# Kernel tuning notes

Hardware: AMD Instinct MI355X
Metric: run time of the kernel (lower is better)

The kernel has to match this reference:

```python
import jax, jax.numpy as jnp
import numpy as np

DIM = 128
H = 8
HD = DIM // H
NL = 6
DFF = 2048
EPS = 1e-5
S2S_STEPS = 6


def _ln(x, g, b):
    m = jnp.mean(x, -1, keepdims=True)
    v = jnp.mean(jnp.square(x - m), -1, keepdims=True)
    return (x - m) / jnp.sqrt(v + EPS) * g + b


def _lstm_step(x, h, c, wih, whh, bih, bhh):
    # torch LSTM gate order: i, f, g, o
    gates = x @ wih.T + bih + h @ whh.T + bhh
    i, f, g, o = jnp.split(gates, 4, axis=-1)
    c = jax.nn.sigmoid(f) * c + jax.nn.sigmoid(i) * jnp.tanh(g)
    h = jax.nn.sigmoid(o) * jnp.tanh(c)
    return h, c


def setup_inputs() -> dict:
    key = jax.random.key(0)
    ks = iter(jax.random.split(key, 16))
    n = lambda shape: jax.random.normal(next(ks), shape, jnp.float32) * 0.02
    inp = {
        "data": jax.random.normal(next(ks), (64, 256, 3), jnp.float32),
        "lin0_w": n((DIM, 3)), "lin0_b": jnp.zeros((DIM,), jnp.float32),
        "attn_in_w": n((NL, 3 * DIM, DIM)), "attn_in_b": jnp.zeros((NL, 3 * DIM), jnp.float32),
        "attn_out_w": n((NL, DIM, DIM)), "attn_out_b": jnp.zeros((NL, DIM), jnp.float32),
        "ln1_g": jnp.ones((NL, DIM), jnp.float32), "ln1_b": jnp.zeros((NL, DIM), jnp.float32),
        "ff_w1": n((NL, DFF, DIM)), "ff_b1": jnp.zeros((NL, DFF), jnp.float32),
        "ff_w2": n((NL, DIM, DFF)), "ff_b2": jnp.zeros((NL, DIM), jnp.float32),
        "ln2_g": jnp.ones((NL, DIM), jnp.float32), "ln2_b": jnp.zeros((NL, DIM), jnp.float32),
        "s2s_wih": n((4 * DIM, 2 * DIM)), "s2s_whh": n((4 * DIM, DIM)),
        "s2s_bih": jnp.zeros((4 * DIM,), jnp.float32), "s2s_bhh": jnp.zeros((4 * DIM,), jnp.float32),
        "mem_wih": n((4 * DIM, 2 * DIM)), "mem_whh": n((4 * DIM, DIM)),
        "mem_bih": jnp.zeros((4 * DIM,), jnp.float32), "mem_bhh": jnp.zeros((4 * DIM,), jnp.float32),
        "lin1_w": n((DIM, DIM)), "lin1_b": jnp.zeros((DIM,), jnp.float32),
        "lin3_w": n((1, DIM)), "lin3_b": jnp.zeros((1,), jnp.float32),
    }
    return inp


def reference(data, lin0_w, lin0_b, attn_in_w, attn_in_b, attn_out_w, attn_out_b,
              ln1_g, ln1_b, ff_w1, ff_b1, ff_w2, ff_b2, ln2_g, ln2_b,
              s2s_wih, s2s_whh, s2s_bih, s2s_bhh,
              mem_wih, mem_whh, mem_bih, mem_bhh,
              lin1_w, lin1_b, lin3_w, lin3_b):
    x = jax.nn.relu(data @ lin0_w.T + lin0_b)  # [S=64, B=256, D]
    S, B, _ = x.shape
    # torch TransformerEncoder with batch_first=False: attention over axis 0,
    # axis 1 is the transformer batch. Post-norm layers (norm_first=False), relu FFN.
    for l in range(NL):
        qkv = x @ attn_in_w[l].T + attn_in_b[l]
        q, k, v = jnp.split(qkv, 3, axis=-1)
        q = q.reshape(S, B, H, HD)
        k = k.reshape(S, B, H, HD)
        v = v.reshape(S, B, H, HD)
        scores = jnp.einsum('sbhd,tbhd->bhst', q, k) / np.float32(np.sqrt(HD))
        attn = jax.nn.softmax(scores, axis=-1)
        ao = jnp.einsum('bhst,tbhd->sbhd', attn, v).reshape(S, B, DIM)
        x = _ln(x + ao @ attn_out_w[l].T + attn_out_b[l], ln1_g[l], ln1_b[l])
        ff = jax.nn.relu(x @ ff_w1[l].T + ff_b1[l]) @ ff_w2[l].T + ff_b2[l]
        x = _ln(x + ff, ln2_g[l], ln2_b[l])
    # Set2Set pooling: bidxs assign segment = axis-0 index for each block of
    # num_atoms consecutive rows of flatten(out,0,1), i.e. pool over axis 1.
    q_star = jnp.zeros((S, 2 * DIM), x.dtype)
    h = jnp.zeros((S, DIM), x.dtype)
    c = jnp.zeros((S, DIM), x.dtype)
    for _ in range(S2S_STEPS):
        h, c = _lstm_step(q_star, h, c, s2s_wih, s2s_whh, s2s_bih, s2s_bhh)
        e = jnp.einsum('bnd,bd->bn', x, h)          # [S, num_atoms]
        a = jax.nn.softmax(e, axis=-1)              # segment softmax (uniform segs)
        r = jnp.einsum('bn,bnd->bd', a, x)          # segment weighted sum
        q_star = jnp.concatenate([h, r], axis=-1)   # [S, 2D]
    # memory LSTM: seq_len 1, zero initial state (states=None branch)
    hx = jnp.zeros((S, DIM), x.dtype)
    cx = jnp.zeros((S, DIM), x.dtype)
    hx, cx = _lstm_step(q_star, hx, cx, mem_wih, mem_whh, mem_bih, mem_bhh)
    o = jax.nn.relu(hx @ lin1_w.T + lin1_b)
    v_out = (o @ lin3_w.T + lin3_b)[None]  # [1, S, 1]
    return v_out, hx[None], cx[None]
```

## Files before the change

### kernel.cpp

```cpp
#include <hip/hip_runtime.h>
#include <math.h>


typedef _Float16 __attribute__((ext_vector_type(8))) f16x8;
typedef __attribute__((ext_vector_type(4))) float f32x4;
typedef _Float16 __attribute__((ext_vector_type(2))) h16x2;

__device__ __forceinline__ unsigned short f2h(float f) {
  union { _Float16 h; unsigned short s; } x; x.h = (_Float16)f; return x.s;
}
__device__ __forceinline__ float h2f(unsigned short u) {
  union { unsigned short s; _Float16 h; } x; x.s = u; return (float)x.h;
}
__device__ __forceinline__ unsigned packh(float a, float b) {
  return (unsigned)f2h(a) | ((unsigned)f2h(b) << 16);
}
__device__ __forceinline__ uint2 pk4(float a, float b, float c, float d) {
  return make_uint2(packh(a, b), packh(c, d));
}
__device__ __forceinline__ float hlo(unsigned u) {
  union { unsigned short s; _Float16 h; } x; x.s = (unsigned short)(u & 0xffff);
  return (float)x.h;
}
__device__ __forceinline__ float hhi(unsigned u) {
  union { unsigned short s; _Float16 h; } x; x.s = (unsigned short)(u >> 16);
  return (float)x.h;
}
__device__ __forceinline__ float fdot2u(unsigned a, unsigned b, float c) {
#if __has_builtin(__builtin_amdgcn_fdot2)
  union U { unsigned u; h16x2 h; };
  U x, y; x.u = a; y.u = b;
  return __builtin_amdgcn_fdot2(x.h, y.h, c, false);
#else
  return c + hlo(a) * hlo(b) + hhi(a) * hhi(b);
#endif
}
__device__ __forceinline__ float sigf(float x) { return 1.f / (1.f + expf(-x)); }

__device__ __forceinline__ void gl2lds16(const void* g, void* l) {
  __builtin_amdgcn_global_load_lds(
      (const __attribute__((address_space(1))) unsigned int*)g,
      (__attribute__((address_space(3))) unsigned int*)l, 16, 0, 0);
}

__global__ __launch_bounds__(256) void convw_kernel(
    const float* __restrict__ aiw, const float* __restrict__ aow,
    const float* __restrict__ w1, const float* __restrict__ w2,
    const float* __restrict__ wih, const float* __restrict__ whh,
    const float* __restrict__ mwih,
    unsigned short* __restrict__ o0, unsigned short* __restrict__ o1,
    unsigned short* __restrict__ o2, unsigned short* __restrict__ o3,
    unsigned short* __restrict__ o4, unsigned short* __restrict__ o5,
    unsigned short* __restrict__ o6) {
  int i = blockIdx.x * 256 + threadIdx.x;
  if (i < 294912) {
    int l = i / 49152, o = i % 49152;
    int j = o & 7, fr = (o >> 3) & 15, fq = (o >> 7) & 3, ks = (o >> 9) & 3,
        rb = o >> 11;
    o0[i] = f2h(aiw[l * 49152 + (rb * 16 + fr) * 128 + ks * 32 + fq * 8 + j]);
  } else if (i < 393216) {
    int ii = i - 294912;
    int l = ii / 16384, o = ii % 16384;
    int j = o & 7, fr = (o >> 3) & 15, fq = (o >> 7) & 3, ks = (o >> 9) & 3,
        rb = o >> 11;
    o1[ii] = f2h(aow[l * 16384 + (rb * 16 + fr) * 128 + ks * 32 + fq * 8 + j]);
  } else if (i < 1966080) {
    int ii = i - 393216;
    int l = ii >> 18, o = ii & 262143;
    int j = o & 7, fr = (o >> 3) & 15, fq = (o >> 7) & 3, ks = (o >> 9) & 3,
        rb = o >> 11;
    o2[ii] = f2h(w1[l * 262144 + (rb * 16 + fr) * 128 + ks * 32 + fq * 8 + j]);
  } else if (i < 3538944) {
    int ii = i - 1966080;
    int l = ii >> 18, o = ii & 262143;
    int j = o & 7, fr = (o >> 3) & 15, fq = (o >> 7) & 3, ks = (o >> 9) & 63,
        rb = o >> 15;
    o3[ii] = f2h(w2[l * 262144 + (rb * 16 + fr) * 2048 + ks * 32 + fq * 8 + j]);
  } else if (i < 3670016) {
    int j = i - 3538944; o4[j] = f2h(wih[j]);
  } else if (i < 3735552) {
    int j = i - 3670016; o5[j] = f2h(whh[j]);
  } else {
    int j = i - 3735552; o6[j] = f2h(mwih[j]);
  }
}

__global__ __launch_bounds__(256) void lin0_kernel(
    const float* __restrict__ data, const float* __restrict__ w,
    const float* __restrict__ b, float* __restrict__ x,
    unsigned short* __restrict__ xb) {
  int i = blockIdx.x * 256 + threadIdx.x;
  int n = i >> 7, d = i & 127;
  float v = b[d] + data[n * 3 + 0] * w[d * 3 + 0]
                 + data[n * 3 + 1] * w[d * 3 + 1]
                 + data[n * 3 + 2] * w[d * 3 + 2];
  v = fmaxf(v, 0.0f);
  x[i] = v;
  xb[i] = f2h(v);
}

__global__ __launch_bounds__(256, 2) void layer_kernel(
    const unsigned short* __restrict__ xbg,
    const unsigned short* __restrict__ wqkv, const float* __restrict__ bqkv,
    const unsigned short* __restrict__ wout, const float* __restrict__ bout,
    const float* __restrict__ ln1g, const float* __restrict__ ln1b,
    const unsigned short* __restrict__ w1, const float* __restrict__ b1,
    const unsigned short* __restrict__ w2, const float* __restrict__ b2,
    const float* __restrict__ ln2g, const float* __restrict__ ln2b,
    float* __restrict__ xio, unsigned short* __restrict__ xbo) {
  __shared__ __align__(16) unsigned short SM[28672];
  __shared__ float psum[4][32], psq[4][32];
  __shared__ float2 stats[32];
  __shared__ __align__(16) uint4 zchunk;

  unsigned short* Xs = SM;
  unsigned short* Ks = SM + 8192;
  unsigned short* VT = SM + 16384;
  unsigned short* AOs = SM + 16384;
  unsigned short* Qs = SM + 24576;
  unsigned short* Xn = SM + 24576;

  int tid = threadIdx.x, w = tid >> 6, lane = tid & 63;
  int b = blockIdx.x >> 1, half = blockIdx.x & 1;
  int r4 = lane >> 4, cs = lane & 15;
  int fr = lane & 15, fq = lane >> 4;

  if (tid == 0) zchunk = make_uint4(0u, 0u, 0u, 0u);

#pragma unroll
  for (int i = 0; i < 4; i++) {
    int issue = w * 4 + i;
    int row = issue * 4 + r4;
    int g = cs ^ (row & 7);
    gl2lds16(xbg + (size_t)(row * 256 + b) * 128 + g * 8,
             (char*)Xs + issue * 1024);
  }
  __syncthreads();

  {
    f32x4 acc[2][2];
#pragma unroll
    for (int i = 0; i < 2; i++)
#pragma unroll
      for (int j = 0; j < 2; j++) acc[i][j] = (f32x4){0.f, 0.f, 0.f, 0.f};
#pragma unroll
    for (int ks = 0; ks < 4; ks++) {
      f16x8 aw[2];
#pragma unroll
      for (int ni = 0; ni < 2; ni++)
        aw[ni] = *(const f16x8*)(wqkv + (size_t)(w * 2 + ni) * 2048 +
                                 ks * 512 + fq * 128 + fr * 8);
      f16x8 bx[2];
#pragma unroll
      for (int mi2 = 0; mi2 < 2; mi2++) {
        int row = half * 32 + mi2 * 16 + fr;
        int kq = (ks * 4 + fq) ^ (row & 7);
        bx[mi2] = *(const f16x8*)(Xs + row * 128 + kq * 8);
      }
#pragma unroll
      for (int mi2 = 0; mi2 < 2; mi2++)
#pragma unroll
        for (int ni = 0; ni < 2; ni++)
          acc[mi2][ni] = __builtin_amdgcn_mfma_f32_16x16x32_f16(
              aw[ni], bx[mi2], acc[mi2][ni], 0, 0, 0);
    }
#pragma unroll
    for (int ni = 0; ni < 2; ni++) {
      int fb = (w * 2 + ni) * 16 + fq * 4;
      float4 bv = *(const float4*)&bqkv[fb];
#pragma unroll
      for (int mi2 = 0; mi2 < 2; mi2++) {
        int srow = mi2 * 16 + fr;
        *(uint2*)(Qs + srow * 128 + (((fb >> 3) ^ (srow & 7)) << 3) +
                  (fb & 7)) =
            pk4(acc[mi2][ni][0] + bv.x, acc[mi2][ni][1] + bv.y,
                acc[mi2][ni][2] + bv.z, acc[mi2][ni][3] + bv.w);
      }
    }
  }
  {
    f32x4 acc[4][2];
#pragma unroll
    for (int i = 0; i < 4; i++)
#pragma unroll
      for (int j = 0; j < 2; j++) acc[i][j] = (f32x4){0.f, 0.f, 0.f, 0.f};
#pragma unroll
    for (int ks = 0; ks < 4; ks++) {
      f16x8 aw[2];
#pragma unroll
      for (int ni = 0; ni < 2; ni++)
        aw[ni] = *(const f16x8*)(wqkv + (size_t)(8 + w * 2 + ni) * 2048 +
                                 ks * 512 + fq * 128 + fr * 8);
      f16x8 bx[4];
#pragma unroll
      for (int mi = 0; mi < 4; mi++) {
        int row = mi * 16 + fr;
        int kq = (ks * 4 + fq) ^ (row & 7);
        bx[mi] = *(const f16x8*)(Xs + row * 128 + kq * 8);
      }
#pragma unroll
      for (int mi = 0; mi < 4; mi++)
#pragma unroll
        for (int ni = 0; ni < 2; ni++)
          acc[mi][ni] = __builtin_amdgcn_mfma_f32_16x16x32_f16(
              aw[ni], bx[mi], acc[mi][ni], 0, 0, 0);
    }
#pragma unroll
    for (int ni = 0; ni < 2; ni++) {
      int fb = (w * 2 + ni) * 16 + fq * 4;
      float4 bv = *(const float4*)&bqkv[128 + fb];
#pragma unroll
      for (int mi = 0; mi < 4; mi++) {
        int srow = mi * 16 + fr;
        *(uint2*)(Ks + srow * 128 + (((fb >> 3) ^ (srow & 7)) << 3) +
                  (fb & 7)) =
            pk4(acc[mi][ni][0] + bv.x, acc[mi][ni][1] + bv.y,
                acc[mi][ni][2] + bv.z, acc[mi][ni][3] + bv.w);
      }
    }
  }
  {
    f32x4 acc[4][2];
#pragma unroll
    for (int i = 0; i < 4; i++)
#pragma unroll
      for (int j = 0; j < 2; j++) acc[i][j] = (f32x4){0.f, 0.f, 0.f, 0.f};
#pragma unroll
    for (int ks = 0; ks < 4; ks++) {
      f16x8 bw[2];
#pragma unroll
      for (int ni = 0; ni < 2; ni++)
        bw[ni] = *(const f16x8*)(wqkv + (size_t)(16 + w * 2 + ni) * 2048 +
                                 ks * 512 + fq * 128 + fr * 8);
      f16x8 ax[4];
#pragma unroll
      for (int mi = 0; mi < 4; mi++) {
        int row = mi * 16 + fr;
        int kq = (ks * 4 + fq) ^ (row & 7);
        ax[mi] = *(const f16x8*)(Xs + row * 128 + kq * 8);
      }
#pragma unroll
      for (int mi = 0; mi < 4; mi++)
#pragma unroll
        for (int ni = 0; ni < 2; ni++)
          acc[mi][ni] = __builtin_amdgcn_mfma_f32_16x16x32_f16(
              ax[mi], bw[ni], acc[mi][ni], 0, 0, 0);
    }
#pragma unroll
    for (int ni = 0; ni < 2; ni++) {
      int feat = (w * 2 + ni) * 16 + fr;
      float bv = bqkv[256 + feat];
#pragma unroll
      for (int mi = 0; mi < 4; mi++) {
        int sb = mi * 16 + fq * 4;
        *(uint2*)(VT + feat * 64 + (((sb >> 3) ^ (feat & 7)) << 3) +
                  (sb & 7)) =
            pk4(acc[mi][ni][0] + bv, acc[mi][ni][1] + bv,
                acc[mi][ni][2] + bv, acc[mi][ni][3] + bv);
      }
    }
  }
  __syncthreads();

  f32x4 po[2][2];
#pragma unroll
  for (int i = 0; i < 2; i++)
#pragma unroll
    for (int j = 0; j < 2; j++) po[i][j] = (f32x4){0.f, 0.f, 0.f, 0.f};
  {
    unsigned short* Pb = Xs + w * 2048;
#pragma unroll
    for (int hi = 0; hi < 2; hi++) {
      int h = w * 2 + hi;
      f16x8 afH[2], bfH[4];
#pragma unroll
      for (int mi2 = 0; mi2 < 2; mi2++) {
        int qrow = mi2 * 16 + fr;
        const unsigned short* pa =
            (fq < 2) ? (Qs + qrow * 128 + (((h * 2 + fq) ^ (qrow & 7)) << 3))
                     : (const unsigned short*)&zchunk;
        afH[mi2] = *(const f16x8*)pa;
      }
#pragma unroll
      for (int ti = 0; ti < 4; ti++) {
        int trow = ti * 16 + fr;
        const unsigned short* pb =
            (fq < 2) ? (Ks + trow * 128 + (((h * 2 + fq) ^ (trow & 7)) << 3))
                     : (const unsigned short*)&zchunk;
        bfH[ti] = *(const f16x8*)pb;
      }
      f32x4 sc[2][4];
#pragma unroll
      for (int i = 0; i < 2; i++)
#pragma unroll
        for (int j = 0; j < 4; j++) sc[i][j] = (f32x4){0.f, 0.f, 0.f, 0.f};
#pragma unroll
      for (int mi2 = 0; mi2 < 2; mi2++)
#pragma unroll
        for (int ti = 0; ti < 4; ti++)
          sc[mi2][ti] = __builtin_amdgcn_mfma_f32_16x16x32_f16(
              afH[mi2], bfH[ti], sc[mi2][ti], 0, 0, 0);
#pragma unroll
      for (int mi2 = 0; mi2 < 2; mi2++) {
#pragma unroll
        for (int r = 0; r < 4; r++) {
          float m = -1e30f;
#pragma unroll
          for (int ti = 0; ti < 4; ti++) m = fmaxf(m, sc[mi2][ti][r]);
          m = fmaxf(m, __shfl_xor(m, 1, 64));
          m = fmaxf(m, __shfl_xor(m, 2, 64));
          m = fmaxf(m, __shfl_xor(m, 4, 64));
          m = fmaxf(m, __shfl_xor(m, 8, 64));
          m *= 0.25f;
          float ss = 0.f;
#pragma unroll
          for (int ti = 0; ti < 4; ti++) {
            float p = expf(sc[mi2][ti][r] * 0.25f - m);
            sc[mi2][ti][r] = p;
            ss += p;
          }
          ss += __shfl_xor(ss, 1, 64);
          ss += __shfl_xor(ss, 2, 64);
          ss += __shfl_xor(ss, 4, 64);
          ss += __shfl_xor(ss, 8, 64);
          float inv = 1.f / ss;
          int prow = mi2 * 16 + fq * 4 + r;
#pragma unroll
          for (int ti = 0; ti < 4; ti++) {
            int t = ti * 16 + fr;
            Pb[prow * 64 + (((t >> 3) ^ (prow & 7)) << 3) + (t & 7)] =
                f2h(sc[mi2][ti][r] * inv);
          }
        }
      }
#pragma unroll
      for (int ks2 = 0; ks2 < 2; ks2++) {
        f16x8 bp[2], avt;
#pragma unroll
        for (int si2 = 0; si2 < 2; si2++) {
          int prow = si2 * 16 + fr;
          int kq = (ks2 * 4 + fq) ^ (prow & 7);
          bp[si2] = *(const f16x8*)(Pb + prow * 64 + kq * 8);
        }
        {
          int vrow = h * 16 + fr;
          int kq = (ks2 * 4 + fq) ^ (vrow & 7);
          avt = *(const f16x8*)(VT + vrow * 64 + kq * 8);
        }
#pragma unroll
        for (int si2 = 0; si2 < 2; si2++)
          po[hi][si2] = __builtin_amdgcn_mfma_f32_16x16x32_f16(
              avt, bp[si2], po[hi][si2], 0, 0, 0);
      }
    }
  }
  __syncthreads();
#pragma unroll
  for (int hi = 0; hi < 2; hi++) {
    int fb = (w * 2 + hi) * 16 + fq * 4;
#pragma unroll
    for (int si2 = 0; si2 < 2; si2++) {
      int srow = si2 * 16 + fr;
      *(uint2*)(AOs + srow * 128 + (((fb >> 3) ^ (srow & 7)) << 3) +
                (fb & 7)) =
          pk4(po[hi][si2][0], po[hi][si2][1], po[hi][si2][2], po[hi][si2][3]);
    }
  }
  __syncthreads();

  {
    f32x4 acc[2][2];
#pragma unroll
    for (int i = 0; i < 2; i++)
#pragma unroll
      for (int j = 0; j < 2; j++) acc[i][j] = (f32x4){0.f, 0.f, 0.f, 0.f};
#pragma unroll
    for (int ks = 0; ks < 4; ks++) {
      f16x8 aw[2], bao[2];
#pragma unroll
      for (int ni = 0; ni < 2; ni++)
        aw[ni] = *(const f16x8*)(wout + (size_t)(w * 2 + ni) * 2048 +
                                 ks * 512 + fq * 128 + fr * 8);
#pragma unroll
      for (int mi2 = 0; mi2 < 2; mi2++) {
        int row = mi2 * 16 + fr;
        int kq = (ks * 4 + fq) ^ (row & 7);
        bao[mi2] = *(const f16x8*)(AOs + row * 128 + kq * 8);
      }
#pragma unroll
      for (int mi2 = 0; mi2 < 2; mi2++)
#pragma unroll
        for (int ni = 0; ni < 2; ni++)
          acc[mi2][ni] = __builtin_amdgcn_mfma_f32_16x16x32_f16(
              aw[ni], bao[mi2], acc[mi2][ni], 0, 0, 0);
    }
    float v4[2][2][4];
    float psA[2] = {0.f, 0.f}, psQ[2] = {0.f, 0.f};
#pragma unroll
    for (int ni = 0; ni < 2; ni++) {
      int fb = (w * 2 + ni) * 16 + fq * 4;
      float4 bv = *(const float4*)&bout[fb];
#pragma unroll
      for (int mi2 = 0; mi2 < 2; mi2++) {
        int rowg = half * 32 + mi2 * 16 + fr;
        float4 rs = *(const float4*)&xio[(size_t)(rowg * 256 + b) * 128 + fb];
        float t0 = acc[mi2][ni][0] + bv.x + rs.x;
        float t1 = acc[mi2][ni][1] + bv.y + rs.y;
        float t2 = acc[mi2][ni][2] + bv.z + rs.z;
        float t3 = acc[mi2][ni][3] + bv.w + rs.w;
        v4[ni][mi2][0] = t0; v4[ni][mi2][1] = t1;
        v4[ni][mi2][2] = t2; v4[ni][mi2][3] = t3;
        psA[mi2] += (t0 + t1) + (t2 + t3);
        psQ[mi2] += (t0 * t0 + t1 * t1) + (t2 * t2 + t3 * t3);
      }
    }
#pragma unroll
    for (int mi2 = 0; mi2 < 2; mi2++) {
      psA[mi2] += __shfl_xor(psA[mi2], 16, 64);
      psA[mi2] += __shfl_xor(psA[mi2], 32, 64);
      psQ[mi2] += __shfl_xor(psQ[mi2], 16, 64);
      psQ[mi2] += __shfl_xor(psQ[mi2], 32, 64);
    }
    if (fq == 0) {
#pragma unroll
      for (int mi2 = 0; mi2 < 2; mi2++) {
        psum[w][mi2 * 16 + fr] = psA[mi2];
        psq[w][mi2 * 16 + fr] = psQ[mi2];
      }
    }
    __syncthreads();
    if (tid < 32) {
      float S = 0.f, Q = 0.f;
#pragma unroll
      for (int ww = 0; ww < 4; ww++) { S += psum[ww][tid]; Q += psq[ww][tid]; }
      float m = S * (1.f / 128.f);
      float var = Q * (1.f / 128.f) - m * m;
      stats[tid] = make_float2(m, rsqrtf(var + 1e-5f));
    }
    __syncthreads();
#pragma unroll
    for (int ni = 0; ni < 2; ni++) {
      int fb = (w * 2 + ni) * 16 + fq * 4;
      float4 g4 = *(const float4*)&ln1g[fb];
      float4 b4 = *(const float4*)&ln1b[fb];
#pragma unroll
      for (int mi2 = 0; mi2 < 2; mi2++) {
        int srow = mi2 * 16 + fr;
        float2 st = stats[srow];
        float y0 = (v4[ni][mi2][0] - st.x) * st.y * g4.x + b4.x;
        float y1 = (v4[ni][mi2][1] - st.x) * st.y * g4.y + b4.y;
        float y2 = (v4[ni][mi2][2] - st.x) * st.y * g4.z + b4.z;
        float y3 = (v4[ni][mi2][3] - st.x) * st.y * g4.w + b4.w;
        *(uint2*)(Xn + srow * 128 + (((fb >> 3) ^ (srow & 7)) << 3) +
                  (fb & 7)) = pk4(y0, y1, y2, y3);
      }
    }
  }
  __syncthreads();

  f16x8 xfragF[4][2];
#pragma unroll
  for (int ks = 0; ks < 4; ks++)
#pragma unroll
    for (int mi2 = 0; mi2 < 2; mi2++) {
      int rowl = mi2 * 16 + fr;
      int kq = (ks * 4 + fq) ^ (rowl & 7);
      xfragF[ks][mi2] = *(const f16x8*)(Xn + rowl * 128 + kq * 8);
    }

  f32x4 acc2[2][2];
#pragma unroll
  for (int i = 0; i < 2; i++)
#pragma unroll
    for (int j = 0; j < 2; j++) acc2[i][j] = (f32x4){0.f, 0.f, 0.f, 0.f};

  for (int c = 0; c < 8; c++) {
    unsigned short* Hcur = SM + (c & 1) * 8192;
    f32x4 acc1[2][4];
#pragma unroll
    for (int i = 0; i < 2; i++)
#pragma unroll
      for (int j = 0; j < 4; j++) acc1[i][j] = (f32x4){0.f, 0.f, 0.f, 0.f};
#pragma unroll
    for (int ks = 0; ks < 4; ks++) {
      f16x8 aw1[4];
#pragma unroll
      for (int ni = 0; ni < 4; ni++)
        aw1[ni] = *(const f16x8*)(w1 + (size_t)(c * 16 + w * 4 + ni) * 2048 +
                                  ks * 512 + fq * 128 + fr * 8);
#pragma unroll
      for (int mi2 = 0; mi2 < 2; mi2++)
#pragma unroll
        for (int ni = 0; ni < 4; ni++)
          acc1[mi2][ni] = __builtin_amdgcn_mfma_f32_16x16x32_f16(
              aw1[ni], xfragF[ks][mi2], acc1[mi2][ni], 0, 0, 0);
    }
#pragma unroll
    for (int ni = 0; ni < 4; ni++) {
      int hb = (w * 4 + ni) * 16 + fq * 4;
      float4 bv = *(const float4*)&b1[c * 256 + hb];
#pragma unroll
      for (int mi2 = 0; mi2 < 2; mi2++) {
        int srow = mi2 * 16 + fr;
        *(uint2*)(Hcur + srow * 256 + (((hb >> 3) ^ (srow & 7)) << 3) +
                  (hb & 7)) =
            pk4(fmaxf(acc1[mi2][ni][0] + bv.x, 0.f),
                fmaxf(acc1[mi2][ni][1] + bv.y, 0.f),
                fmaxf(acc1[mi2][ni][2] + bv.z, 0.f),
                fmaxf(acc1[mi2][ni][3] + bv.w, 0.f));
      }
    }
    __syncthreads();
#pragma unroll
    for (int ks2 = 0; ks2 < 8; ks2++) {
      f16x8 aw2[2], bh[2];
#pragma unroll
      for (int ni = 0; ni < 2; ni++)
        aw2[ni] = *(const f16x8*)(w2 + (size_t)(w * 2 + ni) * 32768 +
                                  (c * 8 + ks2) * 512 + fq * 128 + fr * 8);
#pragma unroll
      for (int mi2 = 0; mi2 < 2; mi2++) {
        int row = mi2 * 16 + fr;
        int kq = (ks2 * 4 + fq) ^ (row & 7);
        bh[mi2] = *(const f16x8*)(Hcur + row * 256 + kq * 8);
      }
#pragma unroll
      for (int mi2 = 0; mi2 < 2; mi2++)
#pragma unroll
        for (int ni = 0; ni < 2; ni++)
          acc2[mi2][ni] = __builtin_amdgcn_mfma_f32_16x16x32_f16(
              aw2[ni], bh[mi2], acc2[mi2][ni], 0, 0, 0);
    }
  }

  {
    float v4[2][2][4];
    float psA[2] = {0.f, 0.f}, psQ[2] = {0.f, 0.f};
#pragma unroll
    for (int ni = 0; ni < 2; ni++) {
      int fb = (w * 2 + ni) * 16 + fq * 4;
      float4 bv = *(const float4*)&b2[fb];
#pragma unroll
      for (int mi2 = 0; mi2 < 2; mi2++) {
        int srow = mi2 * 16 + fr;
        uint2 rz = *(const uint2*)(Xn + srow * 128 +
                                   (((fb >> 3) ^ (srow & 7)) << 3) + (fb & 7));
        float t0 = acc2[mi2][ni][0] + bv.x + hlo(rz.x);
        float t1 = acc2[mi2][ni][1] + bv.y + hhi(rz.x);
        float t2 = acc2[mi2][ni][2] + bv.z + hlo(rz.y);
        float t3 = acc2[mi2][ni][3] + bv.w + hhi(rz.y);
        v4[ni][mi2][0] = t0; v4[ni][mi2][1] = t1;
        v4[ni][mi2][2] = t2; v4[ni][mi2][3] = t3;
        psA[mi2] += (t0 + t1) + (t2 + t3);
        psQ[mi2] += (t0 * t0 + t1 * t1) + (t2 * t2 + t3 * t3);
      }
    }
#pragma unroll
    for (int mi2 = 0; mi2 < 2; mi2++) {
      psA[mi2] += __shfl_xor(psA[mi2], 16, 64);
      psA[mi2] += __shfl_xor(psA[mi2], 32, 64);
      psQ[mi2] += __shfl_xor(psQ[mi2], 16, 64);
      psQ[mi2] += __shfl_xor(psQ[mi2], 32, 64);
    }
    if (fq == 0) {
#pragma unroll
      for (int mi2 = 0; mi2 < 2; mi2++) {
        psum[w][mi2 * 16 + fr] = psA[mi2];
        psq[w][mi2 * 16 + fr] = psQ[mi2];
      }
    }
    __syncthreads();
    if (tid < 32) {
      float S = 0.f, Q = 0.f;
#pragma unroll
      for (int ww = 0; ww < 4; ww++) { S += psum[ww][tid]; Q += psq[ww][tid]; }
      float m = S * (1.f / 128.f);
      float var = Q * (1.f / 128.f) - m * m;
      stats[tid] = make_float2(m, rsqrtf(var + 1e-5f));
    }
    __syncthreads();
#pragma unroll
    for (int ni = 0; ni < 2; ni++) {
      int fb = (w * 2 + ni) * 16 + fq * 4;
      float4 g4 = *(const float4*)&ln2g[fb];
      float4 b4 = *(const float4*)&ln2b[fb];
#pragma unroll
      for (int mi2 = 0; mi2 < 2; mi2++) {
        int srow = mi2 * 16 + fr;
        float2 st = stats[srow];
        float y0 = (v4[ni][mi2][0] - st.x) * st.y * g4.x + b4.x;
        float y1 = (v4[ni][mi2][1] - st.x) * st.y * g4.y + b4.y;
        float y2 = (v4[ni][mi2][2] - st.x) * st.y * g4.z + b4.z;
        float y3 = (v4[ni][mi2][3] - st.x) * st.y * g4.w + b4.w;
        size_t o = (size_t)((half * 32 + srow) * 256 + b) * 128 + fb;
        *(float4*)&xio[o] = make_float4(y0, y1, y2, y3);
        *(uint2*)&xbo[o] = pk4(y0, y1, y2, y3);
      }
    }
  }
}

__global__ __launch_bounds__(512, 1) void s2s_kernel(
    const unsigned short* __restrict__ xb,
    const unsigned short* __restrict__ wihh,
    const unsigned short* __restrict__ whhh,
    const float* __restrict__ bih, const float* __restrict__ bhh,
    const unsigned short* __restrict__ mwihh,
    const float* __restrict__ mbih, const float* __restrict__ mbhh,
    const float* __restrict__ l1w, const float* __restrict__ l1b,
    const float* __restrict__ l3w, const float* __restrict__ l3b,
    float* __restrict__ out) {
  __shared__ __align__(16) unsigned xl[256 * 65];
  __shared__ __align__(16) unsigned qu[128];
  __shared__ __align__(16) float cst[128];
  __shared__ __align__(16) float gates[512];
  __shared__ __align__(16) float red[256];
  __shared__ __align__(16) float aw[256];
  int s = blockIdx.x, t = threadIdx.x, lane = t & 63, w = t >> 6;

  uint4 wreg[32], ureg[16];
  {
    const uint4* wp = (const uint4*)(wihh + (size_t)t * 256);
#pragma unroll
    for (int i = 0; i < 32; i++) wreg[i] = wp[i];
    const uint4* up = (const uint4*)(whhh + (size_t)t * 128);
#pragma unroll
    for (int i = 0; i < 16; i++) ureg[i] = up[i];
  }

  const uint4* xs4 = (const uint4*)(xb + (size_t)s * 32768);
#pragma unroll
  for (int it = 0; it < 8; it++) {
    int f = it * 512 + t;
    uint4 v = xs4[f];
    int n = f >> 4, jc = (f & 15) * 4;
    unsigned* dst = xl + n * 65 + jc;
    dst[0] = v.x; dst[1] = v.y; dst[2] = v.z; dst[3] = v.w;
  }
  if (t < 128) cst[t] = 0.f;
  __syncthreads();

  const uint4* q4 = (const uint4*)qu;
  float bsum = bih[t] + bhh[t];

  for (int step = 0; step < 6; step++) {
    if (step > 0) {
      float a0 = 0.f, a1 = 0.f, a2 = 0.f, a3 = 0.f;
#pragma unroll
      for (int i = 0; i < 16; i++) {
        uint4 qv = q4[i];
        a0 = fdot2u(wreg[i].x, qv.x, a0);
        a1 = fdot2u(wreg[i].y, qv.y, a1);
        a2 = fdot2u(wreg[i].z, qv.z, a2);
        a3 = fdot2u(wreg[i].w, qv.w, a3);
        a0 = fdot2u(ureg[i].x, qv.x, a0);
        a1 = fdot2u(ureg[i].y, qv.y, a1);
        a2 = fdot2u(ureg[i].z, qv.z, a2);
        a3 = fdot2u(ureg[i].w, qv.w, a3);
      }
#pragma unroll
      for (int i = 16; i < 32; i++) {
        uint4 qv = q4[i];
        a0 = fdot2u(wreg[i].x, qv.x, a0);
        a1 = fdot2u(wreg[i].y, qv.y, a1);
        a2 = fdot2u(wreg[i].z, qv.z, a2);
        a3 = fdot2u(wreg[i].w, qv.w, a3);
      }
      gates[t] = bsum + ((a0 + a1) + (a2 + a3));
    } else {
      gates[t] = bsum;
    }
    __syncthreads();
    if (t < 128) {
      float ig = sigf(gates[t]), fg = sigf(gates[128 + t]);
      float gg = tanhf(gates[256 + t]), og = sigf(gates[384 + t]);
      float cn = fg * cst[t] + ig * gg;
      cst[t] = cn;
      float hn = og * tanhf(cn);
      float hp = __shfl_xor(hn, 1, 64);
      if ((t & 1) == 0) qu[t >> 1] = packh(hn, hp);
// ... 66 lines not shown
    gates[t] = mbih[t] + mbhh[t] + ((a0 + a1) + (a2 + a3));
  }
  __syncthreads();
  if (t < 128) {
    float ig = sigf(gates[t]);
    float gg = tanhf(gates[256 + t]);
    float og = sigf(gates[384 + t]);
    float cx = ig * gg;
    float hx = og * tanhf(cx);
    cst[t] = hx;
    out[64 + s * 128 + t] = hx;
    out[64 + 8192 + s * 128 + t] = cx;
  }
  __syncthreads();
  if (t < 128) {
    float acc = l1b[t];
    const float4* w4 = (const float4*)(l1w + (size_t)t * 128);
    const float4* h4 = (const float4*)cst;
#pragma unroll 8
    for (int k = 0; k < 32; k++) {
      float4 a = w4[k], b = h4[k];
      acc += a.x * b.x + a.y * b.y + a.z * b.z + a.w * b.w;
    }
    red[t] = fmaxf(acc, 0.f) * l3w[t];
  } else if (t < 256) {
    red[t] = 0.f;
  }
  __syncthreads();
  for (int off = 128; off; off >>= 1) {
    if (t < off) red[t] += red[t + off];
    __syncthreads();
  }
  if (t == 0) out[s] = red[0] + l3b[0];
}

extern "C" void kernel_launch(void* const* d_in, const int* in_sizes, int n_in,
                              void* d_out, int out_size, void* d_ws,
                              size_t ws_size, hipStream_t stream) {
  const float* data       = (const float*)d_in[0];
  const float* lin0_w     = (const float*)d_in[1];
  const float* lin0_b     = (const float*)d_in[2];
  const float* attn_in_w  = (const float*)d_in[3];
  const float* attn_in_b  = (const float*)d_in[4];
  const float* attn_out_w = (const float*)d_in[5];
  const float* attn_out_b = (const float*)d_in[6];
  const float* ln1_g      = (const float*)d_in[7];
  const float* ln1_b      = (const float*)d_in[8];
  const float* ff_w1      = (const float*)d_in[9];
  const float* ff_b1      = (const float*)d_in[10];
  const float* ff_w2      = (const float*)d_in[11];
  const float* ff_b2      = (const float*)d_in[12];
  const float* ln2_g      = (const float*)d_in[13];
  const float* ln2_b      = (const float*)d_in[14];
  const float* s2s_wih    = (const float*)d_in[15];
  const float* s2s_whh    = (const float*)d_in[16];
  const float* s2s_bih    = (const float*)d_in[17];
  const float* s2s_bhh    = (const float*)d_in[18];
  const float* mem_wih    = (const float*)d_in[19];
  const float* mem_bih    = (const float*)d_in[21];
  const float* mem_bhh    = (const float*)d_in[22];
  const float* lin1_w     = (const float*)d_in[23];
  const float* lin1_b     = (const float*)d_in[24];
  const float* lin3_w     = (const float*)d_in[25];
  const float* lin3_b     = (const float*)d_in[26];
  float* out = (float*)d_out;

  char* p = (char*)d_ws;
  float* x = (float*)p;                      p += (size_t)16384 * 128 * 4;
  unsigned short* xb = (unsigned short*)p;   p += (size_t)16384 * 128 * 2;
  unsigned short* wqkv = (unsigned short*)p; p += (size_t)294912 * 2;
  unsigned short* wout = (unsigned short*)p; p += (size_t)98304 * 2;
  unsigned short* w1h = (unsigned short*)p;  p += (size_t)1572864 * 2;
  unsigned short* w2h = (unsigned short*)p;  p += (size_t)1572864 * 2;
  unsigned short* wihh = (unsigned short*)p; p += (size_t)131072 * 2;
  unsigned short* whhh = (unsigned short*)p; p += (size_t)65536 * 2;
  unsigned short* mwihh = (unsigned short*)p; p += (size_t)131072 * 2;

  convw_kernel<<<15104, 256, 0, stream>>>(
      attn_in_w, attn_out_w, ff_w1, ff_w2, s2s_wih, s2s_whh, mem_wih,
      wqkv, wout, w1h, w2h, wihh, whhh, mwihh);
  lin0_kernel<<<8192, 256, 0, stream>>>(data, lin0_w, lin0_b, x, xb);

  for (int l = 0; l < 6; l++) {
    layer_kernel<<<512, 256, 0, stream>>>(
        xb, wqkv + (size_t)l * 49152, attn_in_b + l * 384,
        wout + (size_t)l * 16384, attn_out_b + l * 128,
        ln1_g + l * 128, ln1_b + l * 128,
        w1h + (size_t)l * 262144, ff_b1 + l * 2048,
        w2h + (size_t)l * 262144, ff_b2 + l * 128,
        ln2_g + l * 128, ln2_b + l * 128, x, xb);
  }

  s2s_kernel<<<64, 512, 0, stream>>>(
      xb, wihh, whhh, s2s_bih, s2s_bhh,
      mwihh, mem_bih, mem_bhh, lin1_w, lin1_b, lin3_w, lin3_b, out);
}
```

Before: 467.1 us.

## Split each batch element's layer across four blocks of 16 query rows

The per-layer kernel now processes 16 query rows per block instead of 32, doubling the grid to 1024 blocks and raising the occupancy target to 3 blocks per CU. Shared memory shrinks and per-thread accumulators halve, which should allow more concurrent blocks and better latency hiding on the 256-CU part. In exchange, each block redundantly recomputes K and V for all 64 tokens and reloads the full FFN weights, so total K/V compute and weight traffic per layer double.

New measurement: 578.2 us. 23.8% more time.

```diff
diff --git a/kernel.cpp b/kernel.cpp
--- a/kernel.cpp
+++ b/kernel.cpp
@@ -99,7 +99,7 @@
   xb[i] = f2h(v);
 }
 
-__global__ __launch_bounds__(256, 2) void layer_kernel(
+__global__ __launch_bounds__(256, 3) void layer_kernel(
     const unsigned short* __restrict__ xbg,
     const unsigned short* __restrict__ wqkv, const float* __restrict__ bqkv,
     const unsigned short* __restrict__ wout, const float* __restrict__ bout,
@@ -108,9 +108,9 @@
     const unsigned short* __restrict__ w2, const float* __restrict__ b2,
     const float* __restrict__ ln2g, const float* __restrict__ ln2b,
     float* __restrict__ xio, unsigned short* __restrict__ xbo) {
-  __shared__ __align__(16) unsigned short SM[28672];
-  __shared__ float psum[4][32], psq[4][32];
-  __shared__ float2 stats[32];
+  __shared__ __align__(16) unsigned short SM[26624];
+  __shared__ float psum[4][16], psq[4][16];
+  __shared__ float2 stats[16];
   __shared__ __align__(16) uint4 zchunk;
 
   unsigned short* Xs = SM;
@@ -121,7 +121,7 @@
   unsigned short* Xn = SM + 24576;
 
   int tid = threadIdx.x, w = tid >> 6, lane = tid & 63;
-  int b = blockIdx.x >> 1, half = blockIdx.x & 1;
+  int b = blockIdx.x >> 2, q = blockIdx.x & 3;
   int r4 = lane >> 4, cs = lane & 15;
   int fr = lane & 15, fq = lane >> 4;
 
@@ -138,11 +138,9 @@
   __syncthreads();
 
   {
-    f32x4 acc[2][2];
-#pragma unroll
-    for (int i = 0; i < 2; i++)
-#pragma unroll
-      for (int j = 0; j < 2; j++) acc[i][j] = (f32x4){0.f, 0.f, 0.f, 0.f};
+    f32x4 acc[2];
+#pragma unroll
+    for (int i = 0; i < 2; i++) acc[i] = (f32x4){0.f, 0.f, 0.f, 0.f};
 #pragma unroll
     for (int ks = 0; ks < 4; ks++) {
       f16x8 aw[2];
@@ -150,32 +148,24 @@
       for (int ni = 0; ni < 2; ni++)
         aw[ni] = *(const f16x8*)(wqkv + (size_t)(w * 2 + ni) * 2048 +
                                  ks * 512 + fq * 128 + fr * 8);
-      f16x8 bx[2];
-#pragma unroll
-      for (int mi2 = 0; mi2 < 2; mi2++) {
-        int row = half * 32 + mi2 * 16 + fr;
+      f16x8 bx;
+      {
+        int row = q * 16 + fr;
         int kq = (ks * 4 + fq) ^ (row & 7);
-        bx[mi2] = *(const f16x8*)(Xs + row * 128 + kq * 8);
-      }
-#pragma unroll
-      for (int mi2 = 0; mi2 < 2; mi2++)
-#pragma unroll
-        for (int ni = 0; ni < 2; ni++)
-          acc[mi2][ni] = __builtin_amdgcn_mfma_f32_16x16x32_f16(
-              aw[ni], bx[mi2], acc[mi2][ni], 0, 0, 0);
+        bx = *(const f16x8*)(Xs + row * 128 + kq * 8);
+      }
+#pragma unroll
+      for (int ni = 0; ni < 2; ni++)
+        acc[ni] = __builtin_amdgcn_mfma_f32_16x16x32_f16(aw[ni], bx, acc[ni],
+                                                         0, 0, 0);
     }
 #pragma unroll
     for (int ni = 0; ni < 2; ni++) {
       int fb = (w * 2 + ni) * 16 + fq * 4;
       float4 bv = *(const float4*)&bqkv[fb];
-#pragma unroll
-      for (int mi2 = 0; mi2 < 2; mi2++) {
-        int srow = mi2 * 16 + fr;
-        *(uint2*)(Qs + srow * 128 + (((fb >> 3) ^ (srow & 7)) << 3) +
-                  (fb & 7)) =
-            pk4(acc[mi2][ni][0] + bv.x, acc[mi2][ni][1] + bv.y,
-                acc[mi2][ni][2] + bv.z, acc[mi2][ni][3] + bv.w);
-      }
+      *(uint2*)(Qs + fr * 128 + (((fb >> 3) ^ (fr & 7)) << 3) + (fb & 7)) =
+          pk4(acc[ni][0] + bv.x, acc[ni][1] + bv.y, acc[ni][2] + bv.z,
+              acc[ni][3] + bv.w);
     }
   }
   {
@@ -262,24 +252,20 @@
   }
   __syncthreads();
 
-  f32x4 po[2][2];
-#pragma unroll
-  for (int i = 0; i < 2; i++)
-#pragma unroll
-    for (int j = 0; j < 2; j++) po[i][j] = (f32x4){0.f, 0.f, 0.f, 0.f};
+  f32x4 po[2];
+#pragma unroll
+  for (int i = 0; i < 2; i++) po[i] = (f32x4){0.f, 0.f, 0.f, 0.f};
   {
-    unsigned short* Pb = Xs + w * 2048;
+    unsigned short* Pb = Xs + w * 1024;
 #pragma unroll
     for (int hi = 0; hi < 2; hi++) {
       int h = w * 2 + hi;
-      f16x8 afH[2], bfH[4];
-#pragma unroll
-      for (int mi2 = 0; mi2 < 2; mi2++) {
-        int qrow = mi2 * 16 + fr;
+      f16x8 afH, bfH[4];
+      {
         const unsigned short* pa =
-            (fq < 2) ? (Qs + qrow * 128 + (((h * 2 + fq) ^ (qrow & 7)) << 3))
+            (fq < 2) ? (Qs + fr * 128 + (((h * 2 + fq) ^ (fr & 7)) << 3))
                      : (const unsigned short*)&zchunk;
-        afH[mi2] = *(const f16x8*)pa;
+        afH = *(const f16x8*)pa;
       }
 #pragma unroll
       for (int ti = 0; ti < 4; ti++) {
@@ -289,68 +275,57 @@
                      : (const unsigned short*)&zchunk;
         bfH[ti] = *(const f16x8*)pb;
       }
-      f32x4 sc[2][4];
-#pragma unroll
-      for (int i = 0; i < 2; i++)
-#pragma unroll
-        for (int j = 0; j < 4; j++) sc[i][j] = (f32x4){0.f, 0.f, 0.f, 0.f};
-#pragma unroll
-      for (int mi2 = 0; mi2 < 2; mi2++)
-#pragma unroll
-        for (int ti = 0; ti < 4; ti++)
-          sc[mi2][ti] = __builtin_amdgcn_mfma_f32_16x16x32_f16(
-              afH[mi2], bfH[ti], sc[mi2][ti], 0, 0, 0);
-#pragma unroll
-      for (int mi2 = 0; mi2 < 2; mi2++) {
-#pragma unroll
-        for (int r = 0; r < 4; r++) {
-          float m = -1e30f;
-#pragma unroll
-          for (int ti = 0; ti < 4; ti++) m = fmaxf(m, sc[mi2][ti][r]);
-          m = fmaxf(m, __shfl_xor(m, 1, 64));
-          m = fmaxf(m, __shfl_xor(m, 2, 64));
-          m = fmaxf(m, __shfl_xor(m, 4, 64));
-          m = fmaxf(m, __shfl_xor(m, 8, 64));
-          m *= 0.25f;
-          float ss = 0.f;
-#pragma unroll
-          for (int ti = 0; ti < 4; ti++) {
-            float p = expf(sc[mi2][ti][r] * 0.25f - m);
-            sc[mi2][ti][r] = p;
-            ss += p;
-          }
-          ss += __shfl_xor(ss, 1, 64);
-          ss += __shfl_xor(ss, 2, 64);
-          ss += __shfl_xor(ss, 4, 64);
-          ss += __shfl_xor(ss, 8, 64);
-          float inv = 1.f / ss;
-          int prow = mi2 * 16 + fq * 4 + r;
-#pragma unroll
-          for (int ti = 0; ti < 4; ti++) {
-            int t = ti * 16 + fr;
-            Pb[prow * 64 + (((t >> 3) ^ (prow & 7)) << 3) + (t & 7)] =
-                f2h(sc[mi2][ti][r] * inv);
-          }
+      f32x4 sc[4];
+#pragma unroll
+      for (int j = 0; j < 4; j++) sc[j] = (f32x4){0.f, 0.f, 0.f, 0.f};
+#pragma unroll
+      for (int ti = 0; ti < 4; ti++)
+        sc[ti] = __builtin_amdgcn_mfma_f32_16x16x32_f16(afH, bfH[ti], sc[ti],
+                                                        0, 0, 0);
+#pragma unroll
+      for (int r = 0; r < 4; r++) {
+        float m = -1e30f;
+#pragma unroll
+        for (int ti = 0; ti < 4; ti++) m = fmaxf(m, sc[ti][r]);
+        m = fmaxf(m, __shfl_xor(m, 1, 64));
+        m = fmaxf(m, __shfl_xor(m, 2, 64));
+        m = fmaxf(m, __shfl_xor(m, 4, 64));
+        m = fmaxf(m, __shfl_xor(m, 8, 64));
+        m *= 0.25f;
+        float ss = 0.f;
+#pragma unroll
+        for (int ti = 0; ti < 4; ti++) {
+          float p = expf(sc[ti][r] * 0.25f - m);
+          sc[ti][r] = p;
+          ss += p;
         }
+        ss += __shfl_xor(ss, 1, 64);
+        ss += __shfl_xor(ss, 2, 64);
+        ss += __shfl_xor(ss, 4, 64);
+        ss += __shfl_xor(ss, 8, 64);
+        float inv = 1.f / ss;
+        int prow = fq * 4 + r;
+#pragma unroll
+        for (int ti = 0; ti < 4; ti++) {
+          int t = ti * 16 + fr;
+          Pb[prow * 64 + (((t >> 3) ^ (prow & 7)) << 3) + (t & 7)] =
+              f2h(sc[ti][r] * inv);
+        }
       }
 #pragma unroll
       for (int ks2 = 0; ks2 < 2; ks2++) {
-        f16x8 bp[2], avt;
-#pragma unroll
-        for (int si2 = 0; si2 < 2; si2++) {
-          int prow = si2 * 16 + fr;
-          int kq = (ks2 * 4 + fq) ^ (prow & 7);
-          bp[si2] = *(const f16x8*)(Pb + prow * 64 + kq * 8);
+        f16x8 bp, avt;
+        {
+          int kq = (ks2 * 4 + fq) ^ (fr & 7);
+          bp = *(const f16x8*)(Pb + fr * 64 + kq * 8);
         }
         {
           int vrow = h * 16 + fr;
           int kq = (ks2 * 4 + fq) ^ (vrow & 7);
           avt = *(const f16x8*)(VT + vrow * 64 + kq * 8);
         }
-#pragma unroll
-        for (int si2 = 0; si2 < 2; si2++)
-          po[hi][si2] = __builtin_amdgcn_mfma_f32_16x16x32_f16(
-              avt, bp[si2], po[hi][si2], 0, 0, 0);
+        po[hi] = __builtin_amdgcn_mfma_f32_16x16x32_f16(avt, bp, po[hi],
+                                                        0, 0, 0);
       }
     }
   }
@@ -358,78 +333,54 @@
 #pragma unroll
   for (int hi = 0; hi < 2; hi++) {
     int fb = (w * 2 + hi) * 16 + fq * 4;
-#pragma unroll
-    for (int si2 = 0; si2 < 2; si2++) {
-      int srow = si2 * 16 + fr;
-      *(uint2*)(AOs + srow * 128 + (((fb >> 3) ^ (srow & 7)) << 3) +
-                (fb & 7)) =
-          pk4(po[hi][si2][0], po[hi][si2][1], po[hi][si2][2], po[hi][si2][3]);
-    }
+    *(uint2*)(AOs + fr * 128 + (((fb >> 3) ^ (fr & 7)) << 3) + (fb & 7)) =
+        pk4(po[hi][0], po[hi][1], po[hi][2], po[hi][3]);
   }
   __syncthreads();
 
   {
-    f32x4 acc[2][2];
-#pragma unroll
-    for (int i = 0; i < 2; i++)
-#pragma unroll
-      for (int j = 0; j < 2; j++) acc[i][j] = (f32x4){0.f, 0.f, 0.f, 0.f};
+    f32x4 acc[2];
+#pragma unroll
+    for (int i = 0; i < 2; i++) acc[i] = (f32x4){0.f, 0.f, 0.f, 0.f};
 #pragma unroll
     for (int ks = 0; ks < 4; ks++) {
-      f16x8 aw[2], bao[2];
+      f16x8 aw[2], bao;
 #pragma unroll
       for (int ni = 0; ni < 2; ni++)
         aw[ni] = *(const f16x8*)(wout + (size_t)(w * 2 + ni) * 2048 +
                                  ks * 512 + fq * 128 + fr * 8);
-#pragma unroll
-      for (int mi2 = 0; mi2 < 2; mi2++) {
-        int row = mi2 * 16 + fr;
-        int kq = (ks * 4 + fq) ^ (row & 7);
-        bao[mi2] = *(const f16x8*)(AOs + row * 128 + kq * 8);
-      }
-#pragma unroll
-      for (int mi2 = 0; mi2 < 2; mi2++)
-#pragma unroll
-        for (int ni = 0; ni < 2; ni++)
-          acc[mi2][ni] = __builtin_amdgcn_mfma_f32_16x16x32_f16(
-              aw[ni], bao[mi2], acc[mi2][ni], 0, 0, 0);
-    }
-    float v4[2][2][4];
-    float psA[2] = {0.f, 0.f}, psQ[2] = {0.f, 0.f};
+      {
+        int kq = (ks * 4 + fq) ^ (fr & 7);
+        bao = *(const f16x8*)(AOs + fr * 128 + kq * 8);
+      }
+#pragma unroll
+      for (int ni = 0; ni < 2; ni++)
+        acc[ni] = __builtin_amdgcn_mfma_f32_16x16x32_f16(aw[ni], bao, acc[ni],
+                                                         0, 0, 0);
+    }
+    float v4[2][4];
+    float psA = 0.f, psQ = 0.f;
+    int rowg = q * 16 + fr;
 #pragma unroll
     for (int ni = 0; ni < 2; ni++) {
       int fb = (w * 2 + ni) * 16 + fq * 4;
       float4 bv = *(const float4*)&bout[fb];
-#pragma unroll
-      for (int mi2 = 0; mi2 < 2; mi2++) {
-        int rowg = half * 32 + mi2 * 16 + fr;
-        float4 rs = *(const float4*)&xio[(size_t)(rowg * 256 + b) * 128 + fb];
-        float t0 = acc[mi2][ni][0] + bv.x + rs.x;
-        float t1 = acc[mi2][ni][1] + bv.y + rs.y;
-        float t2 = acc[mi2][ni][2] + bv.z + rs.z;
-        float t3 = acc[mi2][ni][3] + bv.w + rs.w;
-        v4[ni][mi2][0] = t0; v4[ni][mi2][1] = t1;
-        v4[ni][mi2][2] = t2; v4[ni][mi2][3] = t3;
-        psA[mi2] += (t0 + t1) + (t2 + t3);
-        psQ[mi2] += (t0 * t0 + t1 * t1) + (t2 * t2 + t3 * t3);
-      }
-    }
-#pragma unroll
-    for (int mi2 = 0; mi2 < 2; mi2++) {
-      psA[mi2] += __shfl_xor(psA[mi2], 16, 64);
-      psA[mi2] += __shfl_xor(psA[mi2], 32, 64);
-      psQ[mi2] += __shfl_xor(psQ[mi2], 16, 64);
-      psQ[mi2] += __shfl_xor(psQ[mi2], 32, 64);
-    }
-    if (fq == 0) {
-#pragma unroll
-      for (int mi2 = 0; mi2 < 2; mi2++) {
-        psum[w][mi2 * 16 + fr] = psA[mi2];
-        psq[w][mi2 * 16 + fr] = psQ[mi2];
-      }
-    }
-    __syncthreads();
-    if (tid < 32) {
+      float4 rs = *(const float4*)&xio[(size_t)(rowg * 256 + b) * 128 + fb];
+      float t0 = acc[ni][0] + bv.x + rs.x;
+      float t1 = acc[ni][1] + bv.y + rs.y;
+      float t2 = acc[ni][2] + bv.z + rs.z;
+      float t3 = acc[ni][3] + bv.w + rs.w;
+      v4[ni][0] = t0; v4[ni][1] = t1; v4[ni][2] = t2; v4[ni][3] = t3;
+      psA += (t0 + t1) + (t2 + t3);
+      psQ += (t0 * t0 + t1 * t1) + (t2 * t2 + t3 * t3);
+    }
+    psA += __shfl_xor(psA, 16, 64);
+    psA += __shfl_xor(psA, 32, 64);
+    psQ += __shfl_xor(psQ, 16, 64);
+    psQ += __shfl_xor(psQ, 32, 64);
+    if (fq == 0) { psum[w][fr] = psA; psq[w][fr] = psQ; }
+    __syncthreads();
+    if (tid < 16) {
       float S = 0.f, Q = 0.f;
 #pragma unroll
       for (int ww = 0; ww < 4; ww++) { S += psum[ww][tid]; Q += psq[ww][tid]; }
@@ -438,49 +389,38 @@
       stats[tid] = make_float2(m, rsqrtf(var + 1e-5f));
     }
     __syncthreads();
+    float2 st = stats[fr];
 #pragma unroll
     for (int ni = 0; ni < 2; ni++) {
       int fb = (w * 2 + ni) * 16 + fq * 4;
       float4 g4 = *(const float4*)&ln1g[fb];
       float4 b4 = *(const float4*)&ln1b[fb];
-#pragma unroll
-      for (int mi2 = 0; mi2 < 2; mi2++) {
-        int srow = mi2 * 16 + fr;
-        float2 st = stats[srow];
-        float y0 = (v4[ni][mi2][0] - st.x) * st.y * g4.x + b4.x;
-        float y1 = (v4[ni][mi2][1] - st.x) * st.y * g4.y + b4.y;
-        float y2 = (v4[ni][mi2][2] - st.x) * st.y * g4.z + b4.z;
-        float y3 = (v4[ni][mi2][3] - st.x) * st.y * g4.w + b4.w;
-        *(uint2*)(Xn + srow * 128 + (((fb >> 3) ^ (srow & 7)) << 3) +
-                  (fb & 7)) = pk4(y0, y1, y2, y3);
-      }
-    }
-  }
-  __syncthreads();
-
-  f16x8 xfragF[4][2];
-#pragma unroll
-  for (int ks = 0; ks < 4; ks++)
-#pragma unroll
-    for (int mi2 = 0; mi2 < 2; mi2++) {
-      int rowl = mi2 * 16 + fr;
-      int kq = (ks * 4 + fq) ^ (rowl & 7);
-      xfragF[ks][mi2] = *(const f16x8*)(Xn + rowl * 128 + kq * 8);
-    }
-
-  f32x4 acc2[2][2];
-#pragma unroll
-  for (int i = 0; i < 2; i++)
-#pragma unroll
-    for (int j = 0; j < 2; j++) acc2[i][j] = (f32x4){0.f, 0.f, 0.f, 0.f};
+      float y0 = (v4[ni][0] - st.x) * st.y * g4.x + b4.x;
+      float y1 = (v4[ni][1] - st.x) * st.y * g4.y + b4.y;
+      float y2 = (v4[ni][2] - st.x) * st.y * g4.z + b4.z;
+      float y3 = (v4[ni][3] - st.x) * st.y * g4.w + b4.w;
+      *(uint2*)(Xn + fr * 128 + (((fb >> 3) ^ (fr & 7)) << 3) + (fb & 7)) =
+          pk4(y0, y1, y2, y3);
+    }
+  }
+  __syncthreads();
+
+  f16x8 xfragF[4];
+#pragma unroll
+  for (int ks = 0; ks < 4; ks++) {
+    int kq = (ks * 4 + fq) ^ (fr & 7);
+    xfragF[ks] = *(const f16x8*)(Xn + fr * 128 + kq * 8);
+  }
+
+  f32x4 acc2[2];
+#pragma unroll
+  for (int i = 0; i < 2; i++) acc2[i] = (f32x4){0.f, 0.f, 0.f, 0.f};
 
   for (int c = 0; c < 8; c++) {
-    unsigned short* Hcur = SM + (c & 1) * 8192;
-    f32x4 acc1[2][4];
-#pragma unroll
-    for (int i = 0; i < 2; i++)
-#pragma unroll
-      for (int j = 0; j < 4; j++) acc1[i][j] = (f32x4){0.f, 0.f, 0.f, 0.f};
+    unsigned short* Hcur = Xs + (c & 1) * 4096;
+    f32x4 acc1[4];
+#pragma unroll
+    for (int j = 0; j < 4; j++) acc1[j] = (f32x4){0.f, 0.f, 0.f, 0.f};
 #pragma unroll
     for (int ks = 0; ks < 4; ks++) {
       f16x8 aw1[4];
@@ -489,88 +429,61 @@
         aw1[ni] = *(const f16x8*)(w1 + (size_t)(c * 16 + w * 4 + ni) * 2048 +
                                   ks * 512 + fq * 128 + fr * 8);
 #pragma unroll
-      for (int mi2 = 0; mi2 < 2; mi2++)
-#pragma unroll
-        for (int ni = 0; ni < 4; ni++)
-          acc1[mi2][ni] = __builtin_amdgcn_mfma_f32_16x16x32_f16(
-              aw1[ni], xfragF[ks][mi2], acc1[mi2][ni], 0, 0, 0);
+      for (int ni = 0; ni < 4; ni++)
+        acc1[ni] = __builtin_amdgcn_mfma_f32_16x16x32_f16(
+            aw1[ni], xfragF[ks], acc1[ni], 0, 0, 0);
     }
 #pragma unroll
     for (int ni = 0; ni < 4; ni++) {
       int hb = (w * 4 + ni) * 16 + fq * 4;
       float4 bv = *(const float4*)&b1[c * 256 + hb];
-#pragma unroll
-      for (int mi2 = 0; mi2 < 2; mi2++) {
-        int srow = mi2 * 16 + fr;
-        *(uint2*)(Hcur + srow * 256 + (((hb >> 3) ^ (srow & 7)) << 3) +
-                  (hb & 7)) =
-            pk4(fmaxf(acc1[mi2][ni][0] + bv.x, 0.f),
-                fmaxf(acc1[mi2][ni][1] + bv.y, 0.f),
-                fmaxf(acc1[mi2][ni][2] + bv.z, 0.f),
-                fmaxf(acc1[mi2][ni][3] + bv.w, 0.f));
-      }
+      *(uint2*)(Hcur + fr * 256 + (((hb >> 3) ^ (fr & 7)) << 3) + (hb & 7)) =
+          pk4(fmaxf(acc1[ni][0] + bv.x, 0.f), fmaxf(acc1[ni][1] + bv.y, 0.f),
+              fmaxf(acc1[ni][2] + bv.z, 0.f), fmaxf(acc1[ni][3] + bv.w, 0.f));
     }
     __syncthreads();
 #pragma unroll
     for (int ks2 = 0; ks2 < 8; ks2++) {
-      f16x8 aw2[2], bh[2];
+      f16x8 aw2[2], bh;
 #pragma unroll
       for (int ni = 0; ni < 2; ni++)
         aw2[ni] = *(const f16x8*)(w2 + (size_t)(w * 2 + ni) * 32768 +
                                   (c * 8 + ks2) * 512 + fq * 128 + fr * 8);
-#pragma unroll
-      for (int mi2 = 0; mi2 < 2; mi2++) {
-        int row = mi2 * 16 + fr;
-        int kq = (ks2 * 4 + fq) ^ (row & 7);
-        bh[mi2] = *(const f16x8*)(Hcur + row * 256 + kq * 8);
-      }
-#pragma unroll
-      for (int mi2 = 0; mi2 < 2; mi2++)
-#pragma unroll
-        for (int ni = 0; ni < 2; ni++)
-          acc2[mi2][ni] = __builtin_amdgcn_mfma_f32_16x16x32_f16(
-              aw2[ni], bh[mi2], acc2[mi2][ni], 0, 0, 0);
+      {
+        int kq = (ks2 * 4 + fq) ^ (fr & 7);
+        bh = *(const f16x8*)(Hcur + fr * 256 + kq * 8);
+      }
+#pragma unroll
+      for (int ni = 0; ni < 2; ni++)
+        acc2[ni] = __builtin_amdgcn_mfma_f32_16x16x32_f16(aw2[ni], bh,
+                                                          acc2[ni], 0, 0, 0);
     }
   }
 
   {
-    float v4[2][2][4];
-    float psA[2] = {0.f, 0.f}, psQ[2] = {0.f, 0.f};
+    float v4[2][4];
+    float psA = 0.f, psQ = 0.f;
 #pragma unroll
     for (int ni = 0; ni < 2; ni++) {
       int fb = (w * 2 + ni) * 16 + fq * 4;
       float4 bv = *(const float4*)&b2[fb];
-#pragma unroll
-      for (int mi2 = 0; mi2 < 2; mi2++) {
-        int srow = mi2 * 16 + fr;
-        uint2 rz = *(const uint2*)(Xn + srow * 128 +
-                                   (((fb >> 3) ^ (srow & 7)) << 3) + (fb & 7));
-        float t0 = acc2[mi2][ni][0] + bv.x + hlo(rz.x);
-        float t1 = acc2[mi2][ni][1] + bv.y + hhi(rz.x);
-        float t2 = acc2[mi2][ni][2] + bv.z + hlo(rz.y);
-        float t3 = acc2[mi2][ni][3] + bv.w + hhi(rz.y);
-        v4[ni][mi2][0] = t0; v4[ni][mi2][1] = t1;
-        v4[ni][mi2][2] = t2; v4[ni][mi2][3] = t3;
-        psA[mi2] += (t0 + t1) + (t2 + t3);
-        psQ[mi2] += (t0 * t0 + t1 * t1) + (t2 * t2 + t3 * t3);
-      }
-    }
-#pragma unroll
-    for (int mi2 = 0; mi2 < 2; mi2++) {
-      psA[mi2] += __shfl_xor(psA[mi2], 16, 64);
-      psA[mi2] += __shfl_xor(psA[mi2], 32, 64);
-      psQ[mi2] += __shfl_xor(psQ[mi2], 16, 64);
-      psQ[mi2] += __shfl_xor(psQ[mi2], 32, 64);
-    }
-    if (fq == 0) {
-#pragma unroll
-      for (int mi2 = 0; mi2 < 2; mi2++) {
-        psum[w][mi2 * 16 + fr] = psA[mi2];
-        psq[w][mi2 * 16 + fr] = psQ[mi2];
-      }
-    }
-    __syncthreads();
-    if (tid < 32) {
+      uint2 rz = *(const uint2*)(Xn + fr * 128 +
+                                 (((fb >> 3) ^ (fr & 7)) << 3) + (fb & 7));
+      float t0 = acc2[ni][0] + bv.x + hlo(rz.x);
+      float t1 = acc2[ni][1] + bv.y + hhi(rz.x);
+      float t2 = acc2[ni][2] + bv.z + hlo(rz.y);
+      float t3 = acc2[ni][3] + bv.w + hhi(rz.y);
+      v4[ni][0] = t0; v4[ni][1] = t1; v4[ni][2] = t2; v4[ni][3] = t3;
+      psA += (t0 + t1) + (t2 + t3);
+      psQ += (t0 * t0 + t1 * t1) + (t2 * t2 + t3 * t3);
+    }
+    psA += __shfl_xor(psA, 16, 64);
+    psA += __shfl_xor(psA, 32, 64);
+    psQ += __shfl_xor(psQ, 16, 64);
+    psQ += __shfl_xor(psQ, 32, 64);
+    if (fq == 0) { psum[w][fr] = psA; psq[w][fr] = psQ; }
+    __syncthreads();
+    if (tid < 16) {
       float S = 0.f, Q = 0.f;
 #pragma unroll
       for (int ww = 0; ww < 4; ww++) { S += psum[ww][tid]; Q += psq[ww][tid]; }
@@ -579,23 +492,20 @@
       stats[tid] = make_float2(m, rsqrtf(var + 1e-5f));
     }
     __syncthreads();
+    float2 st = stats[fr];
+    int rowg = q * 16 + fr;
 #pragma unroll
     for (int ni = 0; ni < 2; ni++) {
       int fb = (w * 2 + ni) * 16 + fq * 4;
       float4 g4 = *(const float4*)&ln2g[fb];
       float4 b4 = *(const float4*)&ln2b[fb];
-#pragma unroll
-      for (int mi2 = 0; mi2 < 2; mi2++) {
-        int srow = mi2 * 16 + fr;
-        float2 st = stats[srow];
-        float y0 = (v4[ni][mi2][0] - st.x) * st.y * g4.x + b4.x;
-        float y1 = (v4[ni][mi2][1] - st.x) * st.y * g4.y + b4.y;
-        float y2 = (v4[ni][mi2][2] - st.x) * st.y * g4.z + b4.z;
-        float y3 = (v4[ni][mi2][3] - st.x) * st.y * g4.w + b4.w;
-        size_t o = (size_t)((half * 32 + srow) * 256 + b) * 128 + fb;
-        *(float4*)&xio[o] = make_float4(y0, y1, y2, y3);
-        *(uint2*)&xbo[o] = pk4(y0, y1, y2, y3);
-      }
+      float y0 = (v4[ni][0] - st.x) * st.y * g4.x + b4.x;
+      float y1 = (v4[ni][1] - st.x) * st.y * g4.y + b4.y;
+      float y2 = (v4[ni][2] - st.x) * st.y * g4.z + b4.z;
+      float y3 = (v4[ni][3] - st.x) * st.y * g4.w + b4.w;
+      size_t o = (size_t)(rowg * 256 + b) * 128 + fb;
+      *(float4*)&xio[o] = make_float4(y0, y1, y2, y3);
+      *(uint2*)&xbo[o] = pk4(y0, y1, y2, y3);
     }
   }
 }
@@ -828,7 +738,7 @@
   lin0_kernel<<<8192, 256, 0, stream>>>(data, lin0_w, lin0_b, x, xb);
 
   for (int l = 0; l < 6; l++) {
-    layer_kernel<<<512, 256, 0, stream>>>(
+    layer_kernel<<<1024, 256, 0, stream>>>(
         xb, wqkv + (size_t)l * 49152, attn_in_b + l * 384,
         wout + (size_t)l * 16384, attn_out_b + l * 128,
         ln1_g + l * 128, ln1_b + l * 128,
```
